# Kernel tuning notes

Measured on AMD Instinct MI355X. Metric: run time of the kernel, lower is better.

The kernel has to match this reference:

```python
import jax, jax.numpy as jnp
import numpy as np
from jax.ops import segment_sum

N_GRAPHS, N_PER = 100, 1000
N = N_GRAPHS * N_PER
DEG = 32
E = N * DEG
RATIO = 0.8
K = int(np.ceil(RATIO * N_PER))  # 800, equal-size graphs -> fixed k
F_IN, F_MID, F_OUT = 128, 16, 256


def setup_inputs() -> dict:
    key = jax.random.key(0)
    ks = jax.random.split(key, 10)
    x = jax.random.normal(ks[0], (N, F_IN), dtype=jnp.float32)
    # intra-graph random edges
    epg = E // N_GRAPHS
    src_l = jax.random.randint(ks[1], (N_GRAPHS, epg), 0, N_PER)
    dst_l = jax.random.randint(ks[2], (N_GRAPHS, epg), 0, N_PER)
    offs = (jnp.arange(N_GRAPHS) * N_PER)[:, None]
    edge_index = jnp.stack([(src_l + offs).reshape(-1), (dst_l + offs).reshape(-1)]).astype(jnp.int32)
    batch = jnp.repeat(jnp.arange(N_GRAPHS, dtype=jnp.int32), N_PER)
    s = lambda fan: 1.0 / np.sqrt(fan)
    W1 = jax.random.normal(ks[3], (F_IN, F_MID), dtype=jnp.float32) * s(F_IN)
    b1 = jnp.zeros((F_MID,), dtype=jnp.float32)
    w_rel = jax.random.normal(ks[4], (F_MID, 1), dtype=jnp.float32) * s(F_MID)
    b_rel = jnp.zeros((1,), dtype=jnp.float32)
    w_root = jax.random.normal(ks[5], (F_MID, 1), dtype=jnp.float32) * s(F_MID)
    W2 = jax.random.normal(ks[6], (F_MID, F_OUT), dtype=jnp.float32) * s(F_MID)
    b2 = jnp.zeros((F_OUT,), dtype=jnp.float32)
    return {"x": x, "edge_index": edge_index, "batch": batch,
            "W1": W1, "b1": b1, "w_rel": w_rel, "b_rel": b_rel,
            "w_root": w_root, "W2": W2, "b2": b2}


def _gcn(x, src, dst, W, b, self_w, ew, n):
    # GCNConv with self-loops: D^{-1/2}(A+I)D^{-1/2} X W + b; masked variant
    deg = segment_sum(ew, dst, num_segments=n) + self_w
    dis = jnp.where(deg > 0, jax.lax.rsqrt(deg), 0.0)
    xw = x @ W
    coef = ew * dis[src] * dis[dst]                       # [E]
    agg = segment_sum(xw[src] * coef[:, None], dst, num_segments=n)
    agg = agg + xw * (self_w * dis * dis)[:, None]        # self-loop term
    return agg + b


def reference(x, edge_index, batch, W1, b1, w_rel, b_rel, w_root, W2, b2):
    src, dst = edge_index[0], edge_index[1]
    ones_n = jnp.ones((N,), dtype=x.dtype)
    ones_e = jnp.ones((src.shape[0],), dtype=x.dtype)
    # conv1 + relu
    h = jax.nn.relu(_gcn(x, src, dst, W1, b1, ones_n, ones_e, N))
    # SAGPooling score: GraphConv(16,1) -> tanh
    agg = segment_sum(h[src], dst, num_segments=N)
    score = jnp.tanh((agg @ w_rel + h @ w_root + b_rel)[:, 0])  # [N]
    # per-graph top-k (equal graph sizes -> fixed K), expressed as node mask
    sc2 = score.reshape(N_GRAPHS, N_PER)
    _, idx = jax.lax.top_k(sc2, K)
    mask = jnp.zeros((N_GRAPHS, N_PER), dtype=x.dtype)
    mask = mask.at[jnp.arange(N_GRAPHS)[:, None], idx].set(1.0).reshape(-1)  # [N]
    h = h * (score * mask)[:, None]                       # x[perm] * score[perm]
    em = mask[src] * mask[dst]                            # filter_adj as edge mask
    # conv2 + relu on surviving nodes only
    h2 = jax.nn.relu(_gcn(h, src, dst, W2, b2, mask, em, N)) * mask[:, None]
    # global mean pool over surviving nodes per graph
    sums = segment_sum(h2, batch, num_segments=N_GRAPHS)
    cnt = segment_sum(mask, batch, num_segments=N_GRAPHS)
    return sums / cnt[:, None]
```

## Files before the change

kernel.cpp:

```cpp
#include <hip/hip_runtime.h>
#include <math.h>

#define N_NODES 100000
#define NG 100
#define N_PER 1000
#define N_EDGES 3200000
#define EPG 32000
#define EPG4 8000
#define EPGP 39008
#define K_TOP 800
#define F_IN 128
#define F_MID 16
#define F_OUT 256
#define SENT 1000
#define GEMM_ROWS 256
#define GEMM_BLOCKS ((N_NODES + GEMM_ROWS - 1) / GEMM_ROWS)

typedef __attribute__((ext_vector_type(8))) short short8;
typedef __attribute__((ext_vector_type(4))) float floatx4;

__device__ __forceinline__ unsigned short f2bf(float x) {
    union { float f; unsigned int u; } c; c.f = x;
    unsigned int u = c.u;
    u = u + 0x7FFF + ((u >> 16) & 1);
    return (unsigned short)(u >> 16);
}
__device__ __forceinline__ float bf2f(unsigned short h) {
    return __uint_as_float(((unsigned int)h) << 16);
}
__device__ __forceinline__ void add4(float4& a, const float4 b) {
    a.x += b.x; a.y += b.y; a.z += b.z; a.w += b.w;
}
__device__ __forceinline__ int fidx4(int s, int l) {
    return s * 16 + ((4 * (l + ((s >> 1) & 3))) & 15);
}
__device__ __forceinline__ unsigned int fkey(float f) {
    unsigned int u = __float_as_uint(f);
    return (u & 0x80000000u) ? ~u : (u | 0x80000000u);
}
__device__ __forceinline__ float unfkey(unsigned int k) {
    return __uint_as_float((k & 0x80000000u) ? (k & 0x7FFFFFFFu) : ~k);
}

__global__ __launch_bounds__(1024) void k_front(const float* __restrict__ x,
    const float* __restrict__ W1, const int* __restrict__ ei,
    unsigned short* __restrict__ csr, int* __restrict__ cnt8G, int* __restrict__ rsG,
    float* __restrict__ dis1G, float* __restrict__ xw1)
{
    __shared__ __align__(16) char smem[16640];
    int b = blockIdx.x, t = threadIdx.x;
    if (b < NG) {
        int* cnts = (int*)smem;
        int* cur  = (int*)(smem + 4000);
        int* rs   = (int*)(smem + 8000);
        int* scan = (int*)(smem + 12000);
        int g = b, ebase = g * EPG, nbase = g * N_PER;
        const int4* dst4 = (const int4*)(ei + N_EDGES + ebase);
        const int4* src4 = (const int4*)(ei + ebase);
        if (t < N_PER) { cnts[t] = 0; cur[t] = 0; }
        __syncthreads();
        for (int i = t; i < EPG4; i += 1024) {
            int4 d = dst4[i];
            atomicAdd(&cnts[d.x - nbase], 1);
            atomicAdd(&cnts[d.y - nbase], 1);
            atomicAdd(&cnts[d.z - nbase], 1);
            atomicAdd(&cnts[d.w - nbase], 1);
        }
        __syncthreads();
        int c = (t < N_PER) ? cnts[t] : 0;
        int c8 = (c + 7) & ~7;
        scan[t] = c8;
        __syncthreads();
        for (int dd = 1; dd < 1024; dd <<= 1) {
            int v = (t >= dd) ? scan[t - dd] : 0;
            __syncthreads();
            scan[t] += v;
            __syncthreads();
        }
        int exc = scan[t] - c8;
        unsigned short* cg = csr + (size_t)g * EPGP;
        if (t < N_PER) {
            rs[t] = exc; rsG[nbase + t] = exc; cnt8G[nbase + t] = c8;
            dis1G[nbase + t] = rsqrtf((float)c + 1.0f);
            for (int q = c; q < c8; q++) cg[exc + q] = (unsigned short)SENT;
        }
        __syncthreads();
        for (int i = t; i < EPG4; i += 1024) {
            int4 s4 = src4[i]; int4 d4 = dst4[i];
            int dl, p;
            dl = d4.x - nbase; p = rs[dl] + atomicAdd(&cur[dl], 1); cg[p] = (unsigned short)(s4.x - nbase);
            dl = d4.y - nbase; p = rs[dl] + atomicAdd(&cur[dl], 1); cg[p] = (unsigned short)(s4.y - nbase);
            dl = d4.z - nbase; p = rs[dl] + atomicAdd(&cur[dl], 1); cg[p] = (unsigned short)(s4.z - nbase);
            dl = d4.w - nbase; p = rs[dl] + atomicAdd(&cur[dl], 1); cg[p] = (unsigned short)(s4.w - nbase);
        }
    } else {
        unsigned short* bTh = (unsigned short*)smem;
        unsigned short* bTl = (unsigned short*)(smem + 4096);
        for (int i = t; i < F_IN * F_MID; i += 1024) {
            int k = i >> 4, n = i & 15;
            float w = W1[i];
            unsigned short hh = f2bf(w);
            bTh[n * 128 + k] = hh;
            bTl[n * 128 + k] = f2bf(w - bf2f(hh));
        }
        __syncthreads();
        int wave = t >> 6, lane = t & 63;
        int m = lane & 15, q = lane >> 4;
        long rbase = (long)(b - NG) * GEMM_ROWS + wave * 16;
        long arow = rbase + m;
        const float* xr = x + ((arow < N_NODES) ? arow : (N_NODES - 1)) * F_IN;
        short8 ah[4], al[4], bh[4], bl[4];
#pragma unroll
        for (int c = 0; c < 4; c++) {
            float4 v0 = *(const float4*)(xr + 32 * c + 8 * q);
            float4 v1 = *(const float4*)(xr + 32 * c + 8 * q + 4);
            float vv[8] = {v0.x, v0.y, v0.z, v0.w, v1.x, v1.y, v1.z, v1.w};
            short8 h8, l8;
#pragma unroll
            for (int i = 0; i < 8; i++) {
                unsigned short hh = f2bf(vv[i]);
                h8[i] = (short)hh;
                l8[i] = (short)f2bf(vv[i] - bf2f(hh));
            }
            ah[c] = h8; al[c] = l8;
            bh[c] = *(const short8*)(bTh + m * 128 + 32 * c + 8 * q);
            bl[c] = *(const short8*)(bTl + m * 128 + 32 * c + 8 * q);
        }
        floatx4 acc = {0.f, 0.f, 0.f, 0.f};
#pragma unroll
        for (int c = 0; c < 4; c++) {
            acc = __builtin_amdgcn_mfma_f32_16x16x32_bf16(ah[c], bh[c], acc, 0, 0, 0);
            acc = __builtin_amdgcn_mfma_f32_16x16x32_bf16(al[c], bh[c], acc, 0, 0, 0);
            acc = __builtin_amdgcn_mfma_f32_16x16x32_bf16(ah[c], bl[c], acc, 0, 0, 0);
        }
#pragma unroll
        for (int r = 0; r < 4; r++) {
            long orow = rbase + q * 4 + r;
            if (orow < N_NODES) xw1[orow * F_MID + m] = acc[r];
        }
    }
}

__global__ __launch_bounds__(1024) void k_mega(const unsigned short* __restrict__ csr,
    const int* __restrict__ cnt8G, const int* __restrict__ rsG,
    const float* __restrict__ dis1G, const float* __restrict__ xw1,
    const float* __restrict__ b1, const float* __restrict__ w_rel,
    const float* __restrict__ b_rel, const float* __restrict__ w_root,
    const float* __restrict__ W2, const float* __restrict__ b2,
    float* __restrict__ out)
{
    __shared__ __align__(16) float feat[(N_PER + 1) * F_MID];
    __shared__ __align__(16) unsigned short fbf[N_PER * F_MID];
    __shared__ __align__(16) unsigned short w2t[F_OUT * F_MID];
    __shared__ float sc[N_PER];
    __shared__ float msk[N_PER + 1];
    __shared__ float wsrc[N_PER + 1];
    __shared__ float hw[N_PER + 1];
    __shared__ float hro[N_PER];
    __shared__ float dis2a[N_PER];
    __shared__ float dis1l[N_PER];
    __shared__ int cnt8l[N_PER];
    __shared__ int rsl[N_PER];
    __shared__ int hist[1024];
    __shared__ float partial[F_OUT];
    __shared__ int wtot[16], wexc[16];
    __shared__ unsigned int tiebits[32];
    __shared__ int sh_b1, sh_r1, sh_len, sh_cntgt;
    __shared__ float sh_thr;

    int t = threadIdx.x, g = blockIdx.x;
    int nbase = g * N_PER;
    const unsigned short* cg = csr + (size_t)g * EPGP;
    int grp = t >> 2, l = t & 3;
    int lane = t & 63, wid = t >> 6;

    if (t < N_PER) { cnt8l[t] = cnt8G[nbase + t]; rsl[t] = rsG[nbase + t]; dis1l[t] = dis1G[nbase + t]; }
    if (t == 0) { sh_cntgt = 0; sh_len = 0; }
    if (t < 32) tiebits[t] = 0;
    for (int i = t; i < F_OUT * F_MID; i += 1024) {
        int f = i >> 4, jj = i & 15;
        w2t[i] = f2bf(W2[jj * F_OUT + f]);
    }
    __syncthreads();

    {
        const float4* xsrc = (const float4*)(xw1 + (size_t)nbase * F_MID);
        for (int i = t; i < N_PER * 4; i += 1024) {
            int n = i >> 2, q = i & 3;
            float4 v = xsrc[i];
            float d = dis1l[n];
            v.x *= d; v.y *= d; v.z *= d; v.w *= d;
            *(float4*)(feat + fidx4(n, q)) = v;
        }
        if (t < 4) { float4 z = {0.f, 0.f, 0.f, 0.f}; *(float4*)(feat + fidx4(SENT, t)) = z; }
    }
    __syncthreads();

    float4 b14 = *(const float4*)(b1 + 4 * l);
    float4 wr4 = *(const float4*)(w_rel + 4 * l);
    float4 wo4 = *(const float4*)(w_root + 4 * l);
    float brel = b_rel[0];

    float4 hreg[4];
#pragma unroll
    for (int rr = 0; rr < 4; rr++) {
        int n = grp + 256 * rr;
        if (n < N_PER) {
            int c8 = cnt8l[n];
            const unsigned short* cp = cg + rsl[n];
            float4 A0 = {0,0,0,0}, A1 = A0, A2 = A0, A3 = A0, A4 = A0, A5 = A0, A6 = A0, A7 = A0;
            for (int k = 0; k < c8; k += 8) {
                uint4 wv = *(const uint4*)(cp + k);
                add4(A0, *(const float4*)(feat + fidx4((int)(wv.x & 0xFFFF), l)));
                add4(A1, *(const float4*)(feat + fidx4((int)(wv.x >> 16), l)));
                add4(A2, *(const float4*)(feat + fidx4((int)(wv.y & 0xFFFF), l)));
                add4(A3, *(const float4*)(feat + fidx4((int)(wv.y >> 16), l)));
                add4(A4, *(const float4*)(feat + fidx4((int)(wv.z & 0xFFFF), l)));
                add4(A5, *(const float4*)(feat + fidx4((int)(wv.z >> 16), l)));
                add4(A6, *(const float4*)(feat + fidx4((int)(wv.w & 0xFFFF), l)));
                add4(A7, *(const float4*)(feat + fidx4((int)(wv.w >> 16), l)));
            }
            add4(A0, A1); add4(A2, A3); add4(A4, A5); add4(A6, A7);
            add4(A0, A2); add4(A4, A6); add4(A0, A4);
            float4 sf = *(const float4*)(feat + fidx4(n, l));
            float di = dis1l[n];
            float4 hv;
            hv.x = fmaxf(fmaf(di, A0.x + sf.x, b14.x), 0.f);
            hv.y = fmaxf(fmaf(di, A0.y + sf.y, b14.y), 0.f);
            hv.z = fmaxf(fmaf(di, A0.z + sf.z, b14.z), 0.f);
            hv.w = fmaxf(fmaf(di, A0.w + sf.w, b14.w), 0.f);
            hreg[rr] = hv;
        }
    }
    __syncthreads();
#pragma unroll
    for (int rr = 0; rr < 4; rr++) {
        int n = grp + 256 * rr;
        if (n < N_PER) *(float4*)(feat + fidx4(n, l)) = hreg[rr];
    }
    __syncthreads();

#pragma unroll
    for (int rr = 0; rr < 4; rr++) {
        int n = grp + 256 * rr;
        if (n < N_PER) {
            float4 hv = *(const float4*)(feat + fidx4(n, l));
            float p1 = hv.x * wr4.x + hv.y * wr4.y + hv.z * wr4.z + hv.w * wr4.w;
            float p2 = hv.x * wo4.x + hv.y * wo4.y + hv.z * wo4.z + hv.w * wo4.w;
            p1 += __shfl_xor(p1, 1); p1 += __shfl_xor(p1, 2);
            p2 += __shfl_xor(p2, 1); p2 += __shfl_xor(p2, 2);
            if (l == 0) { hw[n] = p1; hro[n] = p2; }
        }
    }
    if (t == 0) hw[SENT] = 0.f;
    __syncthreads();

#pragma unroll
    for (int rr = 0; rr < 4; rr++) {
        int n = grp + 256 * rr;
        if (n < N_PER) {
            int c8 = cnt8l[n];
            const unsigned short* cp = cg + rsl[n];
            float s0 = 0.f, s1 = 0.f;
            for (int k = 0; k < c8; k += 8) {
                uint4 wv = *(const uint4*)(cp + k);
                int sa = (l == 0) ? (int)(wv.x & 0xFFFF) : (l == 1) ? (int)(wv.x >> 16)
                       : (l == 2) ? (int)(wv.y & 0xFFFF) : (int)(wv.y >> 16);
                int sb = (l == 0) ? (int)(wv.z & 0xFFFF) : (l == 1) ? (int)(wv.z >> 16)
                       : (l == 2) ? (int)(wv.w & 0xFFFF) : (int)(wv.w >> 16);
                s0 += hw[sa]; s1 += hw[sb];
            }
            float sm = s0 + s1;
            sm += __shfl_xor(sm, 1); sm += __shfl_xor(sm, 2);
            if (l == 0) sc[n] = tanhf(sm + hro[n] + brel);
        }
    }
    __syncthreads();

    unsigned int mykey = 0; int myb = -1;
    if (t < N_PER) { mykey = fkey(sc[t]); myb = (int)(mykey >> 22); }
    hist[t] = 0;
    __syncthreads();
    if (t < N_PER) atomicAdd(&hist[myb], 1);
    __syncthreads();
    {
        int cntb = hist[t];
        int v = cntb;
        for (int off = 1; off < 64; off <<= 1) {
            int u = __shfl_down(v, off, 64);
            if (lane + off < 64) v += u;
        }
        if (lane == 0) wtot[wid] = v;
        __syncthreads();
        if (wid == 0) {
            int wv2 = (lane < 16) ? wtot[lane] : 0;
            int sv = wv2;
            for (int off = 1; off < 16; off <<= 1) {
                int u = __shfl_down(sv, off, 64);
                if (lane + off < 64) sv += u;
            }
            if (lane < 16) wexc[lane] = sv - wv2;
        }
        __syncthreads();
        int S = v + wexc[wid];
        if (S >= K_TOP && S - cntb < K_TOP) { sh_b1 = t; sh_r1 = K_TOP - (S - cntb); }
    }
    __syncthreads();
    if (t < N_PER && myb == sh_b1) { int p = atomicAdd(&sh_len, 1); hist[p] = (int)mykey; }
    __syncthreads();
    {
        int L = sh_len, r1 = sh_r1;
        if (t < L) {
            unsigned int k0 = (unsigned int)hist[t];
            int gcnt = 0, ecnt = 0;
            for (int q2 = 0; q2 < L; q2++) {
                unsigned int kq = (unsigned int)hist[q2];
                gcnt += (kq > k0); ecnt += (kq == k0);
            }
            if (gcnt < r1 && r1 <= gcnt + ecnt) sh_thr = unfkey(k0);
        }
    }
    __syncthreads();
    float thr = sh_thr;

    {
        bool pred = (t < N_PER) && (sc[t] > thr);
        bool tied = (t < N_PER) && (sc[t] == thr);
        unsigned long long bal = __ballot(pred);
        if ((t & 63) == 0) atomicAdd(&sh_cntgt, (int)__popcll(bal));
        if (tied) atomicOr(&tiebits[t >> 5], 1u << (t & 31));
        __syncthreads();
        int need = K_TOP - sh_cntgt;
        if (t < N_PER) {
            float v = sc[t];
            float mm;
            if (v > thr) mm = 1.f;
            else if (v < thr) mm = 0.f;
            else {
                int w = t >> 5;
                int rank = __popc(tiebits[w] & ((1u << (t & 31)) - 1u));
                for (int ww = 0; ww < w; ww++) rank += __popc(tiebits[ww]);
                mm = (rank < need) ? 1.f : 0.f;
            }
            msk[t] = mm;
        }
        if (t == 0) { msk[SENT] = 0.f; wsrc[SENT] = 0.f; }
    }
    __syncthreads();

#pragma unroll
    for (int rr = 0; rr < 4; rr++) {
        int n = grp + 256 * rr;
        if (n < N_PER) {
            int c8 = cnt8l[n];
            const unsigned short* cp = cg + rsl[n];
            float s0 = 0.f, s1 = 0.f;
            for (int k = 0; k < c8; k += 8) {
                uint4 wv = *(const uint4*)(cp + k);
                int sa = (l == 0) ? (int)(wv.x & 0xFFFF) : (l == 1) ? (int)(wv.x >> 16)
                       : (l == 2) ? (int)(wv.y & 0xFFFF) : (int)(wv.y >> 16);
                int sb = (l == 0) ? (int)(wv.z & 0xFFFF) : (l == 1) ? (int)(wv.z >> 16)
                       : (l == 2) ? (int)(wv.w & 0xFFFF) : (int)(wv.w >> 16);
                s0 += msk[sa]; s1 += msk[sb];
            }
            float sm = s0 + s1;
            sm += __shfl_xor(sm, 1); sm += __shfl_xor(sm, 2);
            if (l == 0) {
                float d2 = msk[n] * (sm + 1.f);
                float di = (d2 > 0.f) ? rsqrtf(d2) : 0.f;
                dis2a[n] = di;
                wsrc[n] = sc[n] * msk[n] * di;
            }
        }
    }
    __syncthreads();

    for (int i = t; i < N_PER * 4; i += 1024) {
        int n = i >> 2, q = i & 3;
        float w = wsrc[n];
        float4* p = (float4*)(feat + fidx4(n, q));
        float4 v = *p;
        v.x *= w; v.y *= w; v.z *= w; v.w *= w;
        *p = v;
    }
    __syncthreads();

    float4 preg[4];
#pragma unroll
    for (int rr = 0; rr < 4; rr++) {
        int n = grp + 256 * rr;
        if (n < N_PER) {
            float di = dis2a[n];
            float4 pv = {0,0,0,0};
            if (di != 0.f) {
                int c8 = cnt8l[n];
                const unsigned short* cp = cg + rsl[n];
                float4 A0 = {0,0,0,0}, A1 = A0, A2 = A0, A3 = A0, A4 = A0, A5 = A0, A6 = A0, A7 = A0;
                for (int k = 0; k < c8; k += 8) {
                    uint4 wv = *(const uint4*)(cp + k);
                    add4(A0, *(const float4*)(feat + fidx4((int)(wv.x & 0xFFFF), l)));
                    add4(A1, *(const float4*)(feat + fidx4((int)(wv.x >> 16), l)));
                    add4(A2, *(const float4*)(feat + fidx4((int)(wv.y & 0xFFFF), l)));
                    add4(A3, *(const float4*)(feat + fidx4((int)(wv.y >> 16), l)));
                    add4(A4, *(const float4*)(feat + fidx4((int)(wv.z & 0xFFFF), l)));
                    add4(A5, *(const float4*)(feat + fidx4((int)(wv.z >> 16), l)));
                    add4(A6, *(const float4*)(feat + fidx4((int)(wv.w & 0xFFFF), l)));
                    add4(A7, *(const float4*)(feat + fidx4((int)(wv.w >> 16), l)));
                }
                add4(A0, A1); add4(A2, A3); add4(A4, A5); add4(A6, A7);
                add4(A0, A2); add4(A4, A6); add4(A0, A4);
                float4 sf = *(const float4*)(feat + fidx4(n, l));
                pv.x = di * (A0.x + sf.x);
                pv.y = di * (A0.y + sf.y);
                pv.z = di * (A0.z + sf.z);
                pv.w = di * (A0.w + sf.w);
            }
            preg[rr] = pv;
        }
    }
    __syncthreads();
#pragma unroll
    for (int rr = 0; rr < 4; rr++) {
        int n = grp + 256 * rr;
        if (n < N_PER) *(float4*)(feat + fidx4(n, l)) = preg[rr];
    }
    __syncthreads();

    for (int i = t; i < N_PER * 8; i += 1024) {
        int n = i >> 3, cp2 = (i & 7) * 2;
        int phys = n * 16 + ((cp2 + 4 * ((n >> 1) & 3)) & 15);
        float2 v = *(const float2*)(feat + phys);
        unsigned int pk = (unsigned int)f2bf(v.x) | ((unsigned int)f2bf(v.y) << 16);
        ((unsigned int*)fbf)[i] = pk;
    }
    __syncthreads();

    {
        int q = lane >> 4, fl = lane & 15;
        int half = wid >> 3, wcol = wid & 7;
        int c0 = 32 * wcol + fl, c1 = c0 + 16;
        float b2f0 = b2[c0], b2f1 = b2[c1];
        short8 bfrag0 = {0,0,0,0,0,0,0,0}, bfrag1 = bfrag0;
        if (q < 2) {
            bfrag0 = *(const short8*)(w2t + c0 * F_MID + q * 8);
            bfrag1 = *(const short8*)(w2t + c1 * F_MID + q * 8);
        }
        floatx4 zero = {0.f, 0.f, 0.f, 0.f};
        float acc0 = 0.f, acc1 = 0.f;
        int t0 = half ? 32 : 0, t1 = half ? 63 : 32;
        for (int tile = t0; tile < t1; tile++) {
            short8 afrag = {0,0,0,0,0,0,0,0};
            int na = tile * 16 + fl;
            if (q < 2 && na < N_PER)
                afrag = *(const short8*)(fbf + na * F_MID + q * 8);
            floatx4 d0 = __builtin_amdgcn_mfma_f32_16x16x32_bf16(afrag, bfrag0, zero, 0, 0, 0);
            floatx4 d1 = __builtin_amdgcn_mfma_f32_16x16x32_bf16(afrag, bfrag1, zero, 0, 0, 0);
#pragma unroll
            for (int r = 0; r < 4; r++) {
                int nd = tile * 16 + q * 4 + r;
                if (nd < N_PER) {
                    float m = msk[nd];
                    acc0 += m * fmaxf(d0[r] + b2f0, 0.f);
                    acc1 += m * fmaxf(d1[r] + b2f1, 0.f);
                }
            }
        }
        acc0 += __shfl_xor(acc0, 16); acc0 += __shfl_xor(acc0, 32);
        acc1 += __shfl_xor(acc1, 16); acc1 += __shfl_xor(acc1, 32);
        if (half == 0 && lane < 16) { partial[c0] = acc0; partial[c1] = acc1; }
        __syncthreads();
        if (half == 1 && lane < 16) {
            out[g * F_OUT + c0] = (partial[c0] + acc0) * (1.0f / (float)K_TOP);
            out[g * F_OUT + c1] = (partial[c1] + acc1) * (1.0f / (float)K_TOP);
        }
    }
}

extern "C" void kernel_launch(void* const* d_in, const int* in_sizes, int n_in,
                              void* d_out, int out_size, void* d_ws, size_t ws_size,
                              hipStream_t stream) {
    const float* x      = (const float*)d_in[0];
    const int*   ei     = (const int*)d_in[1];
    const float* W1     = (const float*)d_in[3];
    const float* b1     = (const float*)d_in[4];
    const float* w_rel  = (const float*)d_in[5];
    const float* b_rel  = (const float*)d_in[6];
    const float* w_root = (const float*)d_in[7];
    const float* W2     = (const float*)d_in[8];
    const float* b2     = (const float*)d_in[9];
    float* out = (float*)d_out;

    char* ws = (char*)d_ws;
    size_t o = 0;
    unsigned short* csr = (unsigned short*)(ws + o); o += (size_t)NG * EPGP * sizeof(unsigned short);
    int*   cnt8G = (int*)(ws + o);   o += (size_t)N_NODES * sizeof(int);
    int*   rsG   = (int*)(ws + o);   o += (size_t)N_NODES * sizeof(int);
    float* dis1G = (float*)(ws + o); o += (size_t)N_NODES * sizeof(float);
    float* xw1   = (float*)(ws + o); o += (size_t)N_NODES * F_MID * sizeof(float);

    k_front<<<NG + GEMM_BLOCKS, 1024, 0, stream>>>(x, W1, ei, csr, cnt8G, rsG, dis1G, xw1);
    k_mega<<<NG, 1024, 0, stream>>>(csr, cnt8G, rsG, dis1G, xw1,
                                    b1, w_rel, b_rel, w_root, W2, b2, out);
}
```

Before: 241.8 us.

## Pad CSR rows to 4 instead of 8 and prefetch per-graph CSR

Each node's neighbor list in the per-graph CSR is now padded to a multiple of 4 instead of 8. This cuts sentinel padding entries and the wasted gathers they cause in the four aggregation loops, which now read uint2 chunks with four accumulators. A warm-up loop at kernel start touches the graph's CSR to pull it into cache. The score projection is fused into the first aggregation loop, removing a shared-memory round trip and one barrier. Each loop now has less instruction-level parallelism per iteration.

```diff
diff --git a/kernel.cpp b/kernel.cpp
--- a/kernel.cpp
+++ b/kernel.cpp
@@ -7,7 +7,7 @@
 #define N_EDGES 3200000
 #define EPG 32000
 #define EPG4 8000
-#define EPGP 39008
+#define CSR_G 36000
 #define K_TOP 800
 #define F_IN 128
 #define F_MID 16
@@ -44,7 +44,7 @@
 
 __global__ __launch_bounds__(1024) void k_front(const float* __restrict__ x,
     const float* __restrict__ W1, const int* __restrict__ ei,
-    unsigned short* __restrict__ csr, int* __restrict__ cnt8G, int* __restrict__ rsG,
+    unsigned short* __restrict__ csr, int* __restrict__ cnt4G, int* __restrict__ rsG,
     float* __restrict__ dis1G, float* __restrict__ xw1)
 {
     __shared__ __align__(16) char smem[16640];
@@ -68,8 +68,8 @@
         }
         __syncthreads();
         int c = (t < N_PER) ? cnts[t] : 0;
-        int c8 = (c + 7) & ~7;
-        scan[t] = c8;
+        int c4 = (c + 3) & ~3;
+        scan[t] = c4;
         __syncthreads();
         for (int dd = 1; dd < 1024; dd <<= 1) {
             int v = (t >= dd) ? scan[t - dd] : 0;
@@ -77,12 +77,12 @@
             scan[t] += v;
             __syncthreads();
         }
-        int exc = scan[t] - c8;
-        unsigned short* cg = csr + (size_t)g * EPGP;
+        int exc = scan[t] - c4;
+        unsigned short* cg = csr + (size_t)g * CSR_G;
         if (t < N_PER) {
-            rs[t] = exc; rsG[nbase + t] = exc; cnt8G[nbase + t] = c8;
+            rs[t] = exc; rsG[nbase + t] = exc; cnt4G[nbase + t] = c4;
             dis1G[nbase + t] = rsqrtf((float)c + 1.0f);
-            for (int q = c; q < c8; q++) cg[exc + q] = (unsigned short)SENT;
+            for (int q = c; q < c4; q++) cg[exc + q] = (unsigned short)SENT;
         }
         __syncthreads();
         for (int i = t; i < EPG4; i += 1024) {
@@ -142,7 +142,7 @@
 }
 
 __global__ __launch_bounds__(1024) void k_mega(const unsigned short* __restrict__ csr,
-    const int* __restrict__ cnt8G, const int* __restrict__ rsG,
+    const int* __restrict__ cnt4G, const int* __restrict__ rsG,
     const float* __restrict__ dis1G, const float* __restrict__ xw1,
     const float* __restrict__ b1, const float* __restrict__ w_rel,
     const float* __restrict__ b_rel, const float* __restrict__ w_root,
@@ -159,7 +159,7 @@
     __shared__ float hro[N_PER];
     __shared__ float dis2a[N_PER];
     __shared__ float dis1l[N_PER];
-    __shared__ int cnt8l[N_PER];
+    __shared__ int cnt4l[N_PER];
     __shared__ int rsl[N_PER];
     __shared__ int hist[1024];
     __shared__ float partial[F_OUT];
@@ -170,11 +170,18 @@
 
     int t = threadIdx.x, g = blockIdx.x;
     int nbase = g * N_PER;
-    const unsigned short* cg = csr + (size_t)g * EPGP;
+    const unsigned short* cg = csr + (size_t)g * CSR_G;
     int grp = t >> 2, l = t & 3;
     int lane = t & 63, wid = t >> 6;
 
-    if (t < N_PER) { cnt8l[t] = cnt8G[nbase + t]; rsl[t] = rsG[nbase + t]; dis1l[t] = dis1G[nbase + t]; }
+    {
+        const uint4* pf = (const uint4*)cg;
+        unsigned int acc = 0;
+        for (int i = t; i < 4500; i += 1024) acc |= pf[i].x;
+        asm volatile("" :: "v"(acc));
+    }
+
+    if (t < N_PER) { cnt4l[t] = cnt4G[nbase + t]; rsl[t] = rsG[nbase + t]; dis1l[t] = dis1G[nbase + t]; }
     if (t == 0) { sh_cntgt = 0; sh_len = 0; }
     if (t < 32) tiebits[t] = 0;
     for (int i = t; i < F_OUT * F_MID; i += 1024) {
@@ -193,6 +200,7 @@
             *(float4*)(feat + fidx4(n, q)) = v;
         }
         if (t < 4) { float4 z = {0.f, 0.f, 0.f, 0.f}; *(float4*)(feat + fidx4(SENT, t)) = z; }
+        if (t == 0) { hw[SENT] = 0.f; msk[SENT] = 0.f; wsrc[SENT] = 0.f; }
     }
     __syncthreads();
 
@@ -206,45 +214,25 @@
     for (int rr = 0; rr < 4; rr++) {
         int n = grp + 256 * rr;
         if (n < N_PER) {
-            int c8 = cnt8l[n];
+            int c4 = cnt4l[n];
             const unsigned short* cp = cg + rsl[n];
-            float4 A0 = {0,0,0,0}, A1 = A0, A2 = A0, A3 = A0, A4 = A0, A5 = A0, A6 = A0, A7 = A0;
-            for (int k = 0; k < c8; k += 8) {
-                uint4 wv = *(const uint4*)(cp + k);
-                add4(A0, *(const float4*)(feat + fidx4((int)(wv.x & 0xFFFF), l)));
-                add4(A1, *(const float4*)(feat + fidx4((int)(wv.x >> 16), l)));
-                add4(A2, *(const float4*)(feat + fidx4((int)(wv.y & 0xFFFF), l)));
-                add4(A3, *(const float4*)(feat + fidx4((int)(wv.y >> 16), l)));
-                add4(A4, *(const float4*)(feat + fidx4((int)(wv.z & 0xFFFF), l)));
-                add4(A5, *(const float4*)(feat + fidx4((int)(wv.z >> 16), l)));
-                add4(A6, *(const float4*)(feat + fidx4((int)(wv.w & 0xFFFF), l)));
-                add4(A7, *(const float4*)(feat + fidx4((int)(wv.w >> 16), l)));
-            }
-            add4(A0, A1); add4(A2, A3); add4(A4, A5); add4(A6, A7);
-            add4(A0, A2); add4(A4, A6); add4(A0, A4);
+            float4 a0 = {0,0,0,0}, a1 = a0, a2 = a0, a3 = a0;
+            for (int k = 0; k < c4; k += 4) {
+                uint2 wv = *(const uint2*)(cp + k);
+                add4(a0, *(const float4*)(feat + fidx4((int)(wv.x & 0xFFFF), l)));
+                add4(a1, *(const float4*)(feat + fidx4((int)(wv.x >> 16), l)));
+                add4(a2, *(const float4*)(feat + fidx4((int)(wv.y & 0xFFFF), l)));
+                add4(a3, *(const float4*)(feat + fidx4((int)(wv.y >> 16), l)));
+            }
+            add4(a0, a1); add4(a2, a3); add4(a0, a2);
             float4 sf = *(const float4*)(feat + fidx4(n, l));
             float di = dis1l[n];
             float4 hv;
-            hv.x = fmaxf(fmaf(di, A0.x + sf.x, b14.x), 0.f);
-            hv.y = fmaxf(fmaf(di, A0.y + sf.y, b14.y), 0.f);
-            hv.z = fmaxf(fmaf(di, A0.z + sf.z, b14.z), 0.f);
-            hv.w = fmaxf(fmaf(di, A0.w + sf.w, b14.w), 0.f);
+            hv.x = fmaxf(fmaf(di, a0.x + sf.x, b14.x), 0.f);
+            hv.y = fmaxf(fmaf(di, a0.y + sf.y, b14.y), 0.f);
+            hv.z = fmaxf(fmaf(di, a0.z + sf.z, b14.z), 0.f);
+            hv.w = fmaxf(fmaf(di, a0.w + sf.w, b14.w), 0.f);
             hreg[rr] = hv;
-        }
-    }
-    __syncthreads();
-#pragma unroll
-    for (int rr = 0; rr < 4; rr++) {
-        int n = grp + 256 * rr;
-        if (n < N_PER) *(float4*)(feat + fidx4(n, l)) = hreg[rr];
-    }
-    __syncthreads();
-
-#pragma unroll
-    for (int rr = 0; rr < 4; rr++) {
-        int n = grp + 256 * rr;
-        if (n < N_PER) {
-            float4 hv = *(const float4*)(feat + fidx4(n, l));
             float p1 = hv.x * wr4.x + hv.y * wr4.y + hv.z * wr4.z + hv.w * wr4.w;
             float p2 = hv.x * wo4.x + hv.y * wo4.y + hv.z * wo4.z + hv.w * wo4.w;
             p1 += __shfl_xor(p1, 1); p1 += __shfl_xor(p1, 2);
@@ -252,25 +240,27 @@
             if (l == 0) { hw[n] = p1; hro[n] = p2; }
         }
     }
-    if (t == 0) hw[SENT] = 0.f;
+    __syncthreads();
+#pragma unroll
+    for (int rr = 0; rr < 4; rr++) {
+        int n = grp + 256 * rr;
+        if (n < N_PER) *(float4*)(feat + fidx4(n, l)) = hreg[rr];
+    }
     __syncthreads();
 
 #pragma unroll
     for (int rr = 0; rr < 4; rr++) {
         int n = grp + 256 * rr;
         if (n < N_PER) {
-            int c8 = cnt8l[n];
+            int c4 = cnt4l[n];
             const unsigned short* cp = cg + rsl[n];
-            float s0 = 0.f, s1 = 0.f;
-            for (int k = 0; k < c8; k += 8) {
-                uint4 wv = *(const uint4*)(cp + k);
-                int sa = (l == 0) ? (int)(wv.x & 0xFFFF) : (l == 1) ? (int)(wv.x >> 16)
-                       : (l == 2) ? (int)(wv.y & 0xFFFF) : (int)(wv.y >> 16);
-                int sb = (l == 0) ? (int)(wv.z & 0xFFFF) : (l == 1) ? (int)(wv.z >> 16)
-                       : (l == 2) ? (int)(wv.w & 0xFFFF) : (int)(wv.w >> 16);
-                s0 += hw[sa]; s1 += hw[sb];
-            }
-            float sm = s0 + s1;
+            float sm = 0.f;
+            for (int k = 0; k < c4; k += 4) {
+                uint2 wv = *(const uint2*)(cp + k);
+                int s = (l == 0) ? (int)(wv.x & 0xFFFF) : (l == 1) ? (int)(wv.x >> 16)
+                      : (l == 2) ? (int)(wv.y & 0xFFFF) : (int)(wv.y >> 16);
+                sm += hw[s];
+            }
             sm += __shfl_xor(sm, 1); sm += __shfl_xor(sm, 2);
             if (l == 0) sc[n] = tanhf(sm + hro[n] + brel);
         }
@@ -344,7 +334,6 @@
             }
             msk[t] = mm;
         }
-        if (t == 0) { msk[SENT] = 0.f; wsrc[SENT] = 0.f; }
     }
     __syncthreads();
 
@@ -352,18 +341,15 @@
     for (int rr = 0; rr < 4; rr++) {
         int n = grp + 256 * rr;
         if (n < N_PER) {
-            int c8 = cnt8l[n];
+            int c4 = cnt4l[n];
             const unsigned short* cp = cg + rsl[n];
-            float s0 = 0.f, s1 = 0.f;
-            for (int k = 0; k < c8; k += 8) {
-                uint4 wv = *(const uint4*)(cp + k);
-                int sa = (l == 0) ? (int)(wv.x & 0xFFFF) : (l == 1) ? (int)(wv.x >> 16)
-                       : (l == 2) ? (int)(wv.y & 0xFFFF) : (int)(wv.y >> 16);
-                int sb = (l == 0) ? (int)(wv.z & 0xFFFF) : (l == 1) ? (int)(wv.z >> 16)
-                       : (l == 2) ? (int)(wv.w & 0xFFFF) : (int)(wv.w >> 16);
-                s0 += msk[sa]; s1 += msk[sb];
-            }
-            float sm = s0 + s1;
+            float sm = 0.f;
+            for (int k = 0; k < c4; k += 4) {
+                uint2 wv = *(const uint2*)(cp + k);
+                int s = (l == 0) ? (int)(wv.x & 0xFFFF) : (l == 1) ? (int)(wv.x >> 16)
+                      : (l == 2) ? (int)(wv.y & 0xFFFF) : (int)(wv.y >> 16);
+                sm += msk[s];
+            }
             sm += __shfl_xor(sm, 1); sm += __shfl_xor(sm, 2);
             if (l == 0) {
                 float d2 = msk[n] * (sm + 1.f);
@@ -393,27 +379,22 @@
             float di = dis2a[n];
             float4 pv = {0,0,0,0};
             if (di != 0.f) {
-                int c8 = cnt8l[n];
+                int c4 = cnt4l[n];
                 const unsigned short* cp = cg + rsl[n];
-                float4 A0 = {0,0,0,0}, A1 = A0, A2 = A0, A3 = A0, A4 = A0, A5 = A0, A6 = A0, A7 = A0;
-                for (int k = 0; k < c8; k += 8) {
-                    uint4 wv = *(const uint4*)(cp + k);
-                    add4(A0, *(const float4*)(feat + fidx4((int)(wv.x & 0xFFFF), l)));
-                    add4(A1, *(const float4*)(feat + fidx4((int)(wv.x >> 16), l)));
-                    add4(A2, *(const float4*)(feat + fidx4((int)(wv.y & 0xFFFF), l)));
-                    add4(A3, *(const float4*)(feat + fidx4((int)(wv.y >> 16), l)));
-                    add4(A4, *(const float4*)(feat + fidx4((int)(wv.z & 0xFFFF), l)));
-                    add4(A5, *(const float4*)(feat + fidx4((int)(wv.z >> 16), l)));
-                    add4(A6, *(const float4*)(feat + fidx4((int)(wv.w & 0xFFFF), l)));
-                    add4(A7, *(const float4*)(feat + fidx4((int)(wv.w >> 16), l)));
+                float4 a0 = {0,0,0,0}, a1 = a0, a2 = a0, a3 = a0;
+                for (int k = 0; k < c4; k += 4) {
+                    uint2 wv = *(const uint2*)(cp + k);
+                    add4(a0, *(const float4*)(feat + fidx4((int)(wv.x & 0xFFFF), l)));
+                    add4(a1, *(const float4*)(feat + fidx4((int)(wv.x >> 16), l)));
+                    add4(a2, *(const float4*)(feat + fidx4((int)(wv.y & 0xFFFF), l)));
+                    add4(a3, *(const float4*)(feat + fidx4((int)(wv.y >> 16), l)));
                 }
-                add4(A0, A1); add4(A2, A3); add4(A4, A5); add4(A6, A7);
-                add4(A0, A2); add4(A4, A6); add4(A0, A4);
+                add4(a0, a1); add4(a2, a3); add4(a0, a2);
                 float4 sf = *(const float4*)(feat + fidx4(n, l));
-                pv.x = di * (A0.x + sf.x);
-                pv.y = di * (A0.y + sf.y);
-                pv.z = di * (A0.z + sf.z);
-                pv.w = di * (A0.w + sf.w);
+                pv.x = di * (a0.x + sf.x);
+                pv.y = di * (a0.y + sf.y);
+                pv.z = di * (a0.z + sf.z);
+                pv.w = di * (a0.w + sf.w);
             }
             preg[rr] = pv;
         }
@@ -492,13 +473,13 @@
 
     char* ws = (char*)d_ws;
     size_t o = 0;
-    unsigned short* csr = (unsigned short*)(ws + o); o += (size_t)NG * EPGP * sizeof(unsigned short);
-    int*   cnt8G = (int*)(ws + o);   o += (size_t)N_NODES * sizeof(int);
+    unsigned short* csr = (unsigned short*)(ws + o); o += (size_t)NG * CSR_G * sizeof(unsigned short);
+    int*   cnt4G = (int*)(ws + o);   o += (size_t)N_NODES * sizeof(int);
     int*   rsG   = (int*)(ws + o);   o += (size_t)N_NODES * sizeof(int);
     float* dis1G = (float*)(ws + o); o += (size_t)N_NODES * sizeof(float);
     float* xw1   = (float*)(ws + o); o += (size_t)N_NODES * F_MID * sizeof(float);
 
-    k_front<<<NG + GEMM_BLOCKS, 1024, 0, stream>>>(x, W1, ei, csr, cnt8G, rsG, dis1G, xw1);
-    k_mega<<<NG, 1024, 0, stream>>>(csr, cnt8G, rsG, dis1G, xw1,
+    k_front<<<NG + GEMM_BLOCKS, 1024, 0, stream>>>(x, W1, ei, csr, cnt4G, rsG, dis1G, xw1);
+    k_mega<<<NG, 1024, 0, stream>>>(csr, cnt4G, rsG, dis1G, xw1,
                                     b1, w_rel, b_rel, w_root, W2, b2, out);
 }
```

Result: no change. 241.5 us (-0.1%).
